# Optimization experiments

Measured on AMD Instinct MI355X. Metric: run time of the kernel, lower is better.

Reference implementation:

```python
import jax, jax.numpy as jnp
import numpy as np

NX, NY, NZ = 64, 48, 32          # grid_resolution
N = NX * NY * NZ                 # 98304 grid cells
P = 10                           # neighbors_in_radius
D = 3                            # spatial dims
M = 5                            # num_modes (fourier)
BN = 64                          # base_neurons
BN_IN = 8                        # base_neurons_in (output channels)
IN_FEAT = D * (1 + 2 * M)        # 33


def _linear_init(k, fan_in, fan_out):
    s = 1.0 / np.sqrt(fan_in)
    kw, kb = jax.random.split(k)
    W = jax.random.uniform(kw, (fan_in, fan_out), jnp.float32, -s, s)
    b = jax.random.uniform(kb, (fan_out,), jnp.float32, -s, s)
    return W, b


def setup_inputs() -> dict:
    key = jax.random.key(0)
    ks = jax.random.split(key, 6)
    # neighbor point coordinates gathered by ball query: (b, N, P, 3)
    x = jax.random.normal(ks[0], (1, N, P, D), jnp.float32)
    # regular grid coordinates: (b, nx, ny, nz, 3)
    grid = jax.random.normal(ks[1], (1, NX, NY, NZ, D), jnp.float32)
    # fourier frequency buffer: exp(linspace(0, pi, num_modes))
    freqs = jnp.exp(jnp.linspace(0.0, float(np.pi), M)).astype(jnp.float32)
    W1, b1 = _linear_init(ks[2], IN_FEAT, BN)
    W2, b2 = _linear_init(ks[3], BN, BN // 2)
    W3, b3 = _linear_init(ks[4], BN // 2, BN_IN)
    return dict(x=x, grid=grid, freqs=freqs,
                W1=W1, b1=b1, W2=W2, b2=b2, W3=W3, b3=b3)


def _fourier_encode(coords, freqs):
    # coords: (b, N, P, D), freqs: (F,)
    scaled = coords[..., None, :] * freqs[:, None]          # (b, N, P, F, D)
    b, n, p = coords.shape[:3]
    scaled = scaled.reshape(b, n, p, -1)                    # (b, N, P, F*D)
    return jnp.concatenate([jnp.sin(scaled), jnp.cos(scaled)], axis=-1)


def reference(x, grid, freqs, W1, b1, W2, b2, W3, b3):
    gelu = lambda t: jax.nn.gelu(t, approximate=False)  # torch F.gelu default = exact erf
    # Fourier feature encode neighbor coords: (b, N, P, 33)
    facets = jnp.concatenate([x, _fourier_encode(x, freqs)], axis=-1)
    h = gelu(facets @ W1 + b1)                              # (b, N, P, 64)
    h = gelu(h @ W2 + b2)                                   # (b, N, P, 32)
    h = jnp.tanh(h @ W3 + b3)                               # (b, N, P, 8)
    # mask out padded neighbors (zero coords); original uses x-coordinate channel
    mask = (jnp.abs(x[..., 0:1]) > 1e-6).astype(h.dtype)    # (b, N, P, 1)
    out = jnp.sum(h * mask, axis=2)                         # scatter/aggregate -> (b, N, 8)
    out = out.reshape(out.shape[0], NX, NY, NZ, BN_IN)
    return jnp.transpose(out, (0, 4, 1, 2, 3))              # (b, 8, nx, ny, nz)
```

## Files before the change

kernel.cpp:

```cpp
#include <hip/hip_runtime.h>
#include <math.h>

#define NXD 64
#define NYD 48
#define NZD 32
#define NPT (NXD*NYD*NZD)
#define PN  10
#define MF  5
#define H1  64
#define H2  32
#define H3  8

#define PTS_PER_BLOCK 32
#define CHUNKS 2
#define ROWS_PER_BLOCK (PTS_PER_BLOCK*PN)
#define TILES_PER_WAVE 5

#define INV2PI 0.15915494309189535f

typedef __attribute__((ext_vector_type(8))) _Float16 half8;
typedef __attribute__((ext_vector_type(2))) _Float16 half2v;
typedef __attribute__((ext_vector_type(2))) __fp16   fp16x2;
typedef __attribute__((ext_vector_type(2))) short    shortv2;
typedef __attribute__((ext_vector_type(4))) float    f32x4;

__device__ __forceinline__ half2v cvt_pk_h2(float lo, float hi) {
    fp16x2 p = __builtin_amdgcn_cvt_pkrtz(lo, hi);
    return __builtin_bit_cast(half2v, p);
}

static __device__ const unsigned short kSlotTab[32] = {
  2048,    3,   70,  137,  204,  271, 1042, 1109,
  2561, 1176, 1243, 1310,  516,  583,  650,  717,
  2562,  272, 1043, 1110, 1177, 1244, 1311,  517,
    72,  139,  206,  273, 1044, 1111, 1178, 1245 };

__device__ __forceinline__ _Float16 exp2h(_Float16 v) {
    _Float16 r;
    asm("v_exp_f16 %0, %1" : "=v"(r) : "v"(v));
    return r;
}

#define H2C(v) ((half2v){(_Float16)(v), (_Float16)(v)})

__device__ __forceinline__ half2v gelu_pk(float lo, float hi) {
    const half2v x  = cvt_pk_h2(lo, hi);
    const half2v hx = x * H2C(0.5f);
    half2v th = __builtin_elementwise_max(hx, H2C(-1.7f));
    th = __builtin_elementwise_min(th, H2C(1.7f));
    const half2v u = th * th;
    half2v h = __builtin_elementwise_fma(u, H2C(-0.0026649190f), H2C(0.027104255f));
    h = __builtin_elementwise_fma(u, h, H2C(-0.11827712f));
    h = __builtin_elementwise_fma(u, h, H2C(0.30261872f));
    h = __builtin_elementwise_fma(u, h, H2C(-0.52941544f));
    h = __builtin_elementwise_fma(u, h, H2C(0.797885f));
    const half2v w = th * h;
    return __builtin_elementwise_fma(x, w, hx);
}

__device__ __forceinline__ half2v tanh_pk_masked(float lo, float hi, half2v mkh) {
    half2v t = cvt_pk_h2(lo, hi) * H2C(2.8853901f);
    t = __builtin_elementwise_min(t, H2C(14.0f));
    const _Float16 e0 = exp2h(t[0]);
    const _Float16 e1 = exp2h(t[1]);
    const half2v y = (half2v){e0, e1} + H2C(1.0f);
    const shortv2 rb = (shortv2){(short)0x7800, (short)0x7800} - __builtin_bit_cast(shortv2, y);
    half2v r = __builtin_bit_cast(half2v, rb);
    r = r * __builtin_elementwise_fma(-y, r, H2C(2.0f));
    r = r * __builtin_elementwise_fma(-y, r, H2C(2.0f));
    const half2v th = __builtin_elementwise_fma(r, H2C(-2.0f), H2C(1.0f));
    return th * mkh;
}

__global__ __launch_bounds__(256) void domino_mfma_kernel(
    const float* __restrict__ x,
    const float* __restrict__ freqs,
    const float* __restrict__ W1,
    const float* __restrict__ b1,
    const float* __restrict__ W2,
    const float* __restrict__ b2,
    const float* __restrict__ W3,
    const float* __restrict__ b3,
    float* __restrict__ out)
{
    __shared__ __align__(16) float cbuf[2][976];
    __shared__ __align__(16) _Float16 obuf[ROWS_PER_BLOCK * 10];
    __shared__ __align__(16) float coefA[32];
    __shared__ __align__(16) float coefB[32];
    __shared__ __align__(16) float coefO[32];
    __shared__ __align__(16) float biasT[2][4][44];

    const int tid  = threadIdx.x;
    const int w    = tid >> 6;
    const int lane = tid & 63;
    const int lr   = lane & 15;
    const int lg   = lane >> 4;

    auto stage_coords = [&](int c, int buf) {
        const int row0 = (blockIdx.x*CHUNKS + c) * ROWS_PER_BLOCK + w*(TILES_PER_WAVE*16);
        const int sl = (w == 3 && lane >= 60) ? 59 : lane;
        const float* gsrc = x + (size_t)row0 * 3 + (size_t)sl * 4;
        __builtin_amdgcn_global_load_lds(
            (const __attribute__((address_space(1))) void*)gsrc,
            (__attribute__((address_space(3))) void*)&cbuf[buf][w * 240], 16, 0, 0);
    };

    if (tid < 32) {
        const unsigned e = kSlotTab[tid];
        const int m = (e >> 6) & 7, path = (e >> 9) & 1, ty = (e >> 10) & 3;
        const float fm = freqs[m] * INV2PI;
        coefA[tid] = (ty != 2 && path == 0) ? fm : 0.0f;
        coefB[tid] = (ty != 2 && path == 1) ? fm : 0.0f;
        coefO[tid] = (ty == 1) ? 0.25f : 0.0f;
    }

    if (w == 0 && lr == 0) {
        #pragma unroll
        for (int t1 = 0; t1 < 4; ++t1)
            #pragma unroll
            for (int r = 0; r < 4; ++r) {
                const float bv = b1[t1*16 + lg*4 + r];
                const float wv = W1[32*H1 + t1*16 + lg*4 + r];
                biasT[0][lg][t1*4 + r] = bv;      biasT[1][lg][t1*4 + r] = bv;
                biasT[0][lg][16 + t1*4 + r] = wv; biasT[1][lg][16 + t1*4 + r] = wv;
            }
        #pragma unroll
        for (int t2 = 0; t2 < 2; ++t2)
            #pragma unroll
            for (int r = 0; r < 4; ++r) {
                const float bv = b2[t2*16 + lg*4 + r];
                biasT[0][lg][32 + t2*4 + r] = bv; biasT[1][lg][32 + t2*4 + r] = bv;
            }
        #pragma unroll
        for (int r = 0; r < 4; ++r) {
            const float bv = (lg < 2) ? b3[lg*4 + r] : 0.0f;
            biasT[0][lg][40 + r] = bv; biasT[1][lg][40 + r] = bv;
        }
    }

    stage_coords(0, 0);

    const float f4rev = freqs[4] * INV2PI;
    const float rawf  = (lg < 3) ? 1.0f : 0.0f;

    half8 B1f[4];
    #pragma unroll
    for (int t1 = 0; t1 < 4; ++t1)
        #pragma unroll
        for (int j = 0; j < 8; ++j) {
            const int row = kSlotTab[lg*8 + j] & 63;
            B1f[t1][j] = (_Float16)W1[row*H1 + t1*16 + lr];
        }
    half8 B2f[2][2];
    #pragma unroll
    for (int q = 0; q < 2; ++q)
        #pragma unroll
        for (int t2 = 0; t2 < 2; ++t2)
            #pragma unroll
            for (int j = 0; j < 8; ++j)
                B2f[q][t2][j] = (_Float16)W2[((2*q + (j>>2))*16 + lg*4 + (j&3))*H2 + t2*16 + lr];
    half8 B3f;
    #pragma unroll
    for (int j = 0; j < 8; ++j)
        B3f[j] = (lr < H3) ? (_Float16)W3[((j>>2)*16 + lg*4 + (j&3))*H3 + lr] : (_Float16)0.0f;

    __syncthreads();

    const f32x4 fa0 = *(const f32x4*)&coefA[lg*8];
    const f32x4 fb0 = *(const f32x4*)&coefB[lg*8];
    const f32x4 fo0 = *(const f32x4*)&coefO[lg*8];
    const f32x4 fa1 = *(const f32x4*)&coefA[lg*8 + 4];
    const f32x4 fb1 = *(const f32x4*)&coefB[lg*8 + 4];
    const f32x4 fo1 = *(const f32x4*)&coefO[lg*8 + 4];

    #pragma unroll 1
    for (int c = 0; c < CHUNKS; ++c) {
        if (c + 1 < CHUNKS) stage_coords(c + 1, (c + 1) & 1);
        const float* cbp = &cbuf[c & 1][0];

        #pragma unroll
        for (int t = 0; t < TILES_PER_WAVE; ++t) {
            const float* bT = &biasT[t & 1][lg][0];

            const int cfx = w*240 + (t*16 + lr)*3;
            const float cx = cbp[cfx + 0];
            const float cy = cbp[cfx + 1];
            const float cz = cbp[cfx + 2];
            const float cA = (lg <= 1) ? cx : ((lg == 2) ? cy : cz);
            const float cB = (lg == 0) ? cx : ((lg == 1) ? cy : cz);

            float f0 = __builtin_amdgcn_sinf(__builtin_amdgcn_fractf(cA*fa0[0] + (cB*fb0[0] + fo0[0])));
            float f1 = __builtin_amdgcn_sinf(__builtin_amdgcn_fractf(cA*fa0[1] + (cB*fb0[1] + fo0[1])));
            float f2 = __builtin_amdgcn_sinf(__builtin_amdgcn_fractf(cA*fa0[2] + (cB*fb0[2] + fo0[2])));
            float f3 = __builtin_amdgcn_sinf(__builtin_amdgcn_fractf(cA*fa0[3] + (cB*fb0[3] + fo0[3])));
            float f4 = __builtin_amdgcn_sinf(__builtin_amdgcn_fractf(cA*fa1[0] + (cB*fb1[0] + fo1[0])));
            float f5 = __builtin_amdgcn_sinf(__builtin_amdgcn_fractf(cA*fa1[1] + (cB*fb1[1] + fo1[1])));
            float f6 = __builtin_amdgcn_sinf(__builtin_amdgcn_fractf(cA*fa1[2] + (cB*fb1[2] + fo1[2])));
            float f7 = __builtin_amdgcn_sinf(__builtin_amdgcn_fractf(cA*fa1[3] + (cB*fb1[3] + fo1[3])));
            f0 += rawf * (cB - f0);
            const float v32 = __builtin_amdgcn_sinf(__builtin_amdgcn_fractf(cz * f4rev + 0.25f));

            union { half2v h2[4]; half8 h8; } a1u;
            a1u.h2[0] = cvt_pk_h2(f0, f1);
            a1u.h2[1] = cvt_pk_h2(f2, f3);
            a1u.h2[2] = cvt_pk_h2(f4, f5);
            a1u.h2[3] = cvt_pk_h2(f6, f7);
            const half8 a1 = a1u.h8;

            f32x4 c1[4];
            #pragma unroll
            for (int t1 = 0; t1 < 4; ++t1)
                c1[t1] = __builtin_amdgcn_mfma_f32_16x16x32_f16(B1f[t1], a1, *(const f32x4*)&bT[t1*4], 0, 0, 0);
            #pragma unroll
            for (int t1 = 0; t1 < 4; ++t1) {
                const f32x4 wv = *(const f32x4*)&bT[16 + t1*4];
                #pragma unroll
                for (int r = 0; r < 4; ++r)
                    c1[t1][r] += v32 * wv[r];
            }

            union { half2v h2[4]; half8 h8; } a2u0, a2u1;
            a2u0.h2[0] = gelu_pk(c1[0][0], c1[0][1]);
            a2u0.h2[1] = gelu_pk(c1[0][2], c1[0][3]);
            a2u0.h2[2] = gelu_pk(c1[1][0], c1[1][1]);
            a2u0.h2[3] = gelu_pk(c1[1][2], c1[1][3]);
            a2u1.h2[0] = gelu_pk(c1[2][0], c1[2][1]);
            a2u1.h2[1] = gelu_pk(c1[2][2], c1[2][3]);
            a2u1.h2[2] = gelu_pk(c1[3][0], c1[3][1]);
            a2u1.h2[3] = gelu_pk(c1[3][2], c1[3][3]);

            f32x4 c2[2];
            #pragma unroll
            for (int t2 = 0; t2 < 2; ++t2) {
                f32x4 ci = __builtin_amdgcn_mfma_f32_16x16x32_f16(B2f[0][t2], a2u0.h8, *(const f32x4*)&bT[32 + t2*4], 0, 0, 0);
                c2[t2]   = __builtin_amdgcn_mfma_f32_16x16x32_f16(B2f[1][t2], a2u1.h8, ci, 0, 0, 0);
            }

            union { half2v h2[4]; half8 h8; } a3u;
            a3u.h2[0] = gelu_pk(c2[0][0], c2[0][1]);
            a3u.h2[1] = gelu_pk(c2[0][2], c2[0][3]);
            a3u.h2[2] = gelu_pk(c2[1][0], c2[1][1]);
            a3u.h2[3] = gelu_pk(c2[1][2], c2[1][3]);

            f32x4 c3 = __builtin_amdgcn_mfma_f32_16x16x32_f16(B3f, a3u.h8, *(const f32x4*)&bT[40], 0, 0, 0);
            const float mk = (fabsf(cx) > 1e-6f) ? 1.0f : 0.0f;
            const half2v mkh = cvt_pk_h2(mk, mk);
            const half2v t01 = tanh_pk_masked(c3[0], c3[1], mkh);
            const half2v t23 = tanh_pk_masked(c3[2], c3[3], mkh);
            if (lg < 2) {
                const int base = (w*(TILES_PER_WAVE*16) + t*16 + lr)*10 + lg*4;
                *(half2v*)&obuf[base]     = t01;
                *(half2v*)&obuf[base + 2] = t23;
            }
        }

        __syncthreads();

        {
            const int p  = tid >> 3;
            const int ch = tid & 7;
            float sum = 0.0f;
            #pragma unroll
            for (int i = 0; i < PN; ++i) sum += (float)obuf[(p*PN + i)*10 + ch];
            const int gp = blockIdx.x * (PTS_PER_BLOCK*CHUNKS) + c*PTS_PER_BLOCK + p;
            out[(size_t)ch * NPT + gp] = sum;
        }

        if (c + 1 < CHUNKS) __syncthreads();
    }
}

extern "C" void kernel_launch(void* const* d_in, const int* in_sizes, int n_in,
                              void* d_out, int out_size, void* d_ws, size_t ws_size,
                              hipStream_t stream) {
    const float* x     = (const float*)d_in[0];
    const float* freqs = (const float*)d_in[2];
    const float* W1    = (const float*)d_in[3];
    const float* b1    = (const float*)d_in[4];
    const float* W2    = (const float*)d_in[5];
    const float* b2    = (const float*)d_in[6];
    const float* W3    = (const float*)d_in[7];
    const float* b3    = (const float*)d_in[8];
    float* out = (float*)d_out;

    const int grid = NPT / (PTS_PER_BLOCK * CHUNKS);
    domino_mfma_kernel<<<grid, 256, 0, stream>>>(x, freqs, W1, b1, W2, b2, W3, b3, out);
}
```

Baseline: 113.6 us.

## Switch to single-wave blocks with four chunks and drop block barriers

Each block now has one 64-lane wave that processes four 8-point chunks, instead of four waves processing two 32-point chunks. All __syncthreads calls are removed. Explicit s_waitcnt vmcnt instructions wait for the asynchronous global-to-LDS coordinate loads. This removes barrier stalls and lets each wave reuse its register-held weight fragments over more tiles. The costs are more blocks, less latency hiding inside a block, and reliance on hand-counted vmcnt values, which are fragile if the compiler reorders or adds memory ops.

```diff
diff --git a/kernel.cpp b/kernel.cpp
--- a/kernel.cpp
+++ b/kernel.cpp
@@ -11,10 +11,10 @@
 #define H2  32
 #define H3  8
 
-#define PTS_PER_BLOCK 32
-#define CHUNKS 2
-#define ROWS_PER_BLOCK (PTS_PER_BLOCK*PN)
-#define TILES_PER_WAVE 5
+#define CHUNKS 4
+#define PTS_PER_CHUNK 8
+#define ROWS_PER_CHUNK (PTS_PER_CHUNK*PN)
+#define TILES_PER_CHUNK 5
 
 #define INV2PI 0.15915494309189535f
 
@@ -72,7 +72,7 @@
     return th * mkh;
 }
 
-__global__ __launch_bounds__(256) void domino_mfma_kernel(
+__global__ __launch_bounds__(64) void domino_mfma_kernel(
     const float* __restrict__ x,
     const float* __restrict__ freqs,
     const float* __restrict__ W1,
@@ -83,38 +83,36 @@
     const float* __restrict__ b3,
     float* __restrict__ out)
 {
-    __shared__ __align__(16) float cbuf[2][976];
-    __shared__ __align__(16) _Float16 obuf[ROWS_PER_BLOCK * 10];
+    __shared__ __align__(16) float cbuf[2][256];
+    __shared__ __align__(16) _Float16 obuf[ROWS_PER_CHUNK * 10];
     __shared__ __align__(16) float coefA[32];
     __shared__ __align__(16) float coefB[32];
     __shared__ __align__(16) float coefO[32];
     __shared__ __align__(16) float biasT[2][4][44];
 
-    const int tid  = threadIdx.x;
-    const int w    = tid >> 6;
-    const int lane = tid & 63;
+    const int lane = threadIdx.x;
     const int lr   = lane & 15;
     const int lg   = lane >> 4;
 
     auto stage_coords = [&](int c, int buf) {
-        const int row0 = (blockIdx.x*CHUNKS + c) * ROWS_PER_BLOCK + w*(TILES_PER_WAVE*16);
-        const int sl = (w == 3 && lane >= 60) ? 59 : lane;
+        const int row0 = (blockIdx.x*CHUNKS + c) * ROWS_PER_CHUNK;
+        const int sl = (row0 + ROWS_PER_CHUNK == NPT*PN && lane >= 60) ? 59 : lane;
         const float* gsrc = x + (size_t)row0 * 3 + (size_t)sl * 4;
         __builtin_amdgcn_global_load_lds(
             (const __attribute__((address_space(1))) void*)gsrc,
-            (__attribute__((address_space(3))) void*)&cbuf[buf][w * 240], 16, 0, 0);
+            (__attribute__((address_space(3))) void*)&cbuf[buf][0], 16, 0, 0);
     };
 
-    if (tid < 32) {
-        const unsigned e = kSlotTab[tid];
+    if (lane < 32) {
+        const unsigned e = kSlotTab[lane];
         const int m = (e >> 6) & 7, path = (e >> 9) & 1, ty = (e >> 10) & 3;
         const float fm = freqs[m] * INV2PI;
-        coefA[tid] = (ty != 2 && path == 0) ? fm : 0.0f;
-        coefB[tid] = (ty != 2 && path == 1) ? fm : 0.0f;
-        coefO[tid] = (ty == 1) ? 0.25f : 0.0f;
+        coefA[lane] = (ty != 2 && path == 0) ? fm : 0.0f;
+        coefB[lane] = (ty != 2 && path == 1) ? fm : 0.0f;
+        coefO[lane] = (ty == 1) ? 0.25f : 0.0f;
     }
 
-    if (w == 0 && lr == 0) {
+    if (lr == 0) {
         #pragma unroll
         for (int t1 = 0; t1 < 4; ++t1)
             #pragma unroll
@@ -164,8 +162,6 @@
     for (int j = 0; j < 8; ++j)
         B3f[j] = (lr < H3) ? (_Float16)W3[((j>>2)*16 + lg*4 + (j&3))*H3 + lr] : (_Float16)0.0f;
 
-    __syncthreads();
-
     const f32x4 fa0 = *(const f32x4*)&coefA[lg*8];
     const f32x4 fb0 = *(const f32x4*)&coefB[lg*8];
     const f32x4 fo0 = *(const f32x4*)&coefO[lg*8];
@@ -176,13 +172,18 @@
     #pragma unroll 1
     for (int c = 0; c < CHUNKS; ++c) {
         if (c + 1 < CHUNKS) stage_coords(c + 1, (c + 1) & 1);
+
+        if (c == 0 || c + 1 == CHUNKS) asm volatile("s_waitcnt vmcnt(1)" ::: "memory");
+        else                           asm volatile("s_waitcnt vmcnt(2)" ::: "memory");
+        __builtin_amdgcn_sched_barrier(0);
+
         const float* cbp = &cbuf[c & 1][0];
 
         #pragma unroll
-        for (int t = 0; t < TILES_PER_WAVE; ++t) {
+        for (int t = 0; t < TILES_PER_CHUNK; ++t) {
             const float* bT = &biasT[t & 1][lg][0];
 
-            const int cfx = w*240 + (t*16 + lr)*3;
+            const int cfx = (t*16 + lr)*3;
             const float cx = cbp[cfx + 0];
             const float cy = cbp[cfx + 1];
             const float cz = cbp[cfx + 2];
@@ -248,25 +249,21 @@
             const half2v t01 = tanh_pk_masked(c3[0], c3[1], mkh);
             const half2v t23 = tanh_pk_masked(c3[2], c3[3], mkh);
             if (lg < 2) {
-                const int base = (w*(TILES_PER_WAVE*16) + t*16 + lr)*10 + lg*4;
+                const int base = (t*16 + lr)*10 + lg*4;
                 *(half2v*)&obuf[base]     = t01;
                 *(half2v*)&obuf[base + 2] = t23;
             }
         }
 
-        __syncthreads();
-
         {
-            const int p  = tid >> 3;
-            const int ch = tid & 7;
+            const int p  = lane >> 3;
+            const int ch = lane & 7;
             float sum = 0.0f;
             #pragma unroll
             for (int i = 0; i < PN; ++i) sum += (float)obuf[(p*PN + i)*10 + ch];
-            const int gp = blockIdx.x * (PTS_PER_BLOCK*CHUNKS) + c*PTS_PER_BLOCK + p;
+            const int gp = blockIdx.x * (PTS_PER_CHUNK*CHUNKS) + c*PTS_PER_CHUNK + p;
             out[(size_t)ch * NPT + gp] = sum;
         }
-
-        if (c + 1 < CHUNKS) __syncthreads();
     }
 }
 
@@ -283,6 +280,6 @@
     const float* b3    = (const float*)d_in[8];
     float* out = (float*)d_out;
 
-    const int grid = NPT / (PTS_PER_BLOCK * CHUNKS);
-    domino_mfma_kernel<<<grid, 256, 0, stream>>>(x, freqs, W1, b1, W2, b2, W3, b3, out);
-}
+    const int grid = NPT / (PTS_PER_CHUNK * CHUNKS);
+    domino_mfma_kernel<<<grid, 64, 0, stream>>>(x, freqs, W1, b1, W2, b2, W3, b3, out);
+}
```

Measured after the change: 114.9 us. Within noise of the previous version (+1.1%).
